# Performance work log

Measured on AMD Instinct MI355X. Metric: run time of the kernel, lower is better.

The kernel has to match this reference:

```python
import jax, jax.numpy as jnp
import numpy as np

RADII = (4, 8, 16)
BETA = 0.3
TEMP = 0.07
EPS = 1e-6


def box_filter(x, r):
    """Windowed sum over a (2r+1)x(2r+1) window with zero padding (same as
    F.conv2d with a ones kernel and padding=r), applied to the last two axes.
    Uses cumulative sums (integral image) instead of an explicit convolution."""
    def along(x, axis):
        n = x.shape[axis]
        c = jnp.cumsum(x, axis=axis)
        pad = [(0, 0)] * x.ndim
        pad[axis] = (1, 0)
        c = jnp.pad(c, pad)  # prepend a zero so c[i] = sum of first i elems
        i = jnp.arange(n)
        hi = jnp.clip(i + r + 1, 0, n)
        lo = jnp.clip(i - r, 0, n)
        return jnp.take(c, hi, axis=axis) - jnp.take(c, lo, axis=axis)
    return along(along(x, -2), -1)


def build_prototypes(support_feats, mask_f, anchor_pos, anchor_sample, anchor_radius):
    """mask_f: [S,H,W] float. Returns (local_protos [M,C], local_weights [M], global_proto [C])."""
    fg = mask_f.sum()
    global_proto = (support_feats * mask_f[:, None]).sum((0, 2, 3)) / (fg + EPS)

    masked = support_feats * mask_f[:, None]  # [S,C,H,W]
    means, msums = [], []
    for r in RADII:
        fsum = box_filter(masked, r)              # [S,C,H,W] windowed masked feature sum
        msum = box_filter(mask_f, r)              # [S,H,W]   windowed fg pixel count
        means.append(fsum / (msum[:, None] + EPS))
        msums.append(msum)
    mean = jnp.stack(means)   # [R,S,C,H,W] windowed masked means per radius
    msum = jnp.stack(msums)   # [R,S,H,W]

    y, x = anchor_pos[:, 0], anchor_pos[:, 1]
    local_protos = mean[anchor_radius, anchor_sample, :, y, x]   # [M,C]
    local_weights = msum[anchor_radius, anchor_sample, y, x]     # [M]
    local_weights = local_weights / (local_weights.sum() + EPS)
    return local_protos, local_weights, global_proto


def _l2norm(x, axis):
    n = jnp.sqrt(jnp.sum(x * x, axis=axis, keepdims=True))
    return x / jnp.maximum(n, 1e-12)


def reference(support_feats, support_masks, query_feats, anchor_pos, anchor_sample, anchor_radius):
    mask_f = support_masks.astype(support_feats.dtype)[:, 0]  # [S,H,W]
    protos, weights, gproto = build_prototypes(
        support_feats, mask_f, anchor_pos, anchor_sample, anchor_radius)

    q_norm = _l2norm(query_feats, axis=1)                     # [B,C,H,W]
    g = _l2norm(gproto[None], axis=1)[0]                      # [C]
    s_global = jnp.einsum('bchw,c->bhw', q_norm, g)

    p_norm = _l2norm(protos, axis=1)                          # [M,C]
    sims = jnp.einsum('bchw,mc->bmhw', q_norm, p_norm)        # [B,M,H,W]
    w = weights / (weights.sum() + EPS)
    local_score = jnp.einsum('bmhw,m->bhw', sims, w)

    s_fg = BETA * s_global + (1.0 - BETA) * local_score
    logits = jnp.stack((-s_fg / TEMP, s_fg / TEMP), axis=1)   # [B,2,H,W]
    return logits


def setup_inputs() -> dict:
    key = jax.random.key(0)
    k1, k2, k3, k4, k5, k6 = jax.random.split(key, 6)
    S, C, H, W = 4, 384, 96, 96
    B, M = 8, 64
    return {
        'support_feats': jax.random.normal(k1, (S, C, H, W), dtype=jnp.float32),
        'support_masks': jax.random.randint(k2, (S, 1, H, W), 0, 2, dtype=jnp.int32),
        'query_feats': jax.random.normal(k3, (B, C, H, W), dtype=jnp.float32),
        'anchor_pos': jax.random.randint(k4, (M, 2), 0, H, dtype=jnp.int32),
        'anchor_sample': jax.random.randint(k5, (M,), 0, S, dtype=jnp.int32),
        'anchor_radius': jax.random.randint(k6, (M,), 0, len(RADII), dtype=jnp.int32),
    }
```

## Files before the change

### kernel.cpp

```cpp
#include <hip/hip_runtime.h>
#include <hip/hip_bf16.h>
#include <math.h>

#define S_ 4
#define C_ 384
#define H_ 96
#define W_ 96
#define B_ 8
#define M_ 64
#define HW_ (H_ * W_)
#define EPSV 1e-6f
#define BETA_V 0.3f
#define TEMP_V 0.07f

__device__ __forceinline__ float wave_sum(float v) {
#pragma unroll
    for (int o = 32; o; o >>= 1) v += __shfl_down(v, o, 64);
    return v;
}

__device__ __forceinline__ float block_sum(float v) {
    __shared__ float sm[8];
    int lane = threadIdx.x & 63;
    int wid = threadIdx.x >> 6;
    v = wave_sum(v);
    if (lane == 0) sm[wid] = v;
    __syncthreads();
    int nw = blockDim.x >> 6;
    float r = 0.0f;
    for (int i = 0; i < nw; ++i) r += sm[i];
    __syncthreads();
    return r;
}

__global__ __launch_bounds__(256) void k_gpartial(const float* __restrict__ feats,
                                                  const int* __restrict__ mask,
                                                  float* __restrict__ partial) {
    int sc = blockIdx.x;
    int s = sc / C_;
    const float4* fp = (const float4*)(feats + (size_t)sc * HW_);
    const int4* mp = (const int4*)(mask + (size_t)s * HW_);
    float acc = 0.0f;
    for (int i = threadIdx.x; i < HW_ / 4; i += blockDim.x) {
        float4 f = fp[i];
        int4 m = mp[i];
        acc += f.x * (float)m.x + f.y * (float)m.y + f.z * (float)m.z + f.w * (float)m.w;
    }
    float tot = block_sum(acc);
    if (threadIdx.x == 0) partial[sc] = tot;
}

__global__ __launch_bounds__(256) void k_local(const float* __restrict__ feats,
                                               const int* __restrict__ mask,
                                               const int* __restrict__ pos,
                                               const int* __restrict__ samp,
                                               const int* __restrict__ rad,
                                               float* __restrict__ proto,
                                               float* __restrict__ msum_out) {
    const int CG = C_ / 4;
    int m = blockIdx.x / CG;
    int cg = blockIdx.x % CG;
    int y = pos[2 * m + 0];
    int x = pos[2 * m + 1];
    int s = samp[m];
    int ri = rad[m];
    int r = (ri == 0) ? 4 : (ri == 1) ? 8 : 16;
    int y0 = max(y - r, 0), y1 = min(y + r + 1, H_);
    int x0 = max(x - r, 0), x1 = min(x + r + 1, W_);
    int ww = x1 - x0;
    int n = (y1 - y0) * ww;

    __shared__ float mwin[33 * 33];
    const int* mp = mask + (size_t)s * HW_;
    float macc = 0.0f;
    for (int i = threadIdx.x; i < n; i += blockDim.x) {
        int yy = y0 + i / ww;
        int xx = x0 + i % ww;
        float mv = (float)mp[yy * W_ + xx];
        mwin[i] = mv;
        macc += mv;
    }
    float msum = block_sum(macc);
    if (cg == 0 && threadIdx.x == 0) msum_out[m] = msum;
    float inv = 1.0f / (msum + EPSV);

    int wid = threadIdx.x >> 6;
    int lane = threadIdx.x & 63;
    int c = cg * 4 + wid;
    const float* fp = feats + ((size_t)s * C_ + c) * HW_;
    float acc = 0.0f;
    for (int i = lane; i < n; i += 64) {
        int yy = y0 + i / ww;
        int xx = x0 + i % ww;
        acc += fp[yy * W_ + xx] * mwin[i];
    }
    acc = wave_sum(acc);
    if (lane == 0) proto[m * C_ + c] = acc * inv;
}

__global__ __launch_bounds__(256) void k_finalize(const int* __restrict__ mask,
                                                  const float* __restrict__ partial,
                                                  const float* __restrict__ msum,
                                                  const float* __restrict__ proto,
                                                  float* __restrict__ v) {
    int tid = threadIdx.x;
    int wid = tid >> 6;
    int lane = tid & 63;

    const int4* mp4 = (const int4*)mask;
    float acc = 0.0f;
    for (int i = tid; i < S_ * HW_ / 4; i += blockDim.x) {
        int4 m = mp4[i];
        acc += (float)(m.x + m.y + m.z + m.w);
    }
    float fg = block_sum(acc);
    float invfg = 1.0f / (fg + EPSV);

    __shared__ float gv[C_];
    for (int c = tid; c < C_; c += blockDim.x) {
        float t = 0.0f;
        for (int s = 0; s < S_; ++s) t += partial[s * C_ + c];
        gv[c] = t * invfg;
    }
    __syncthreads();

    float sq = 0.0f;
    for (int c = tid; c < C_; c += blockDim.x) sq += gv[c] * gv[c];
    float gn = block_sum(sq);
    gn = fmaxf(sqrtf(gn), 1e-12f);

    float wa = (tid < M_) ? msum[tid] : 0.0f;
    float T = block_sum(wa);
    float wb = (tid < M_) ? msum[tid] / (T + EPSV) : 0.0f;
    float wsum = block_sum(wb);

    __shared__ float pn[M_];
    for (int m = wid; m < M_; m += 4) {
        float a = 0.0f;
        for (int c = lane; c < C_; c += 64) {
            float p = proto[m * C_ + c];
            a += p * p;
        }
        a = wave_sum(a);
        if (lane == 0) pn[m] = fmaxf(sqrtf(a), 1e-12f);
    }
    __syncthreads();

    __shared__ float wq[M_];
    if (tid < M_) {
        float w = (msum[tid] / (T + EPSV)) / (wsum + EPSV);
        wq[tid] = w / pn[tid];
    }
    __syncthreads();

    for (int c = tid; c < C_; c += blockDim.x) {
        float vl = 0.0f;
        for (int m = 0; m < M_; ++m) vl += wq[m] * proto[m * C_ + c];
        v[c] = BETA_V * (gv[c] / gn) + (1.0f - BETA_V) * vl;
    }
}

__global__ __launch_bounds__(256) void k_score(const float* __restrict__ q,
                                               const float* __restrict__ v,
                                               float* __restrict__ out) {
    __shared__ float vs[C_];
    for (int c = threadIdx.x; c < C_; c += blockDim.x) vs[c] = v[c];
    __syncthreads();

    int wid = threadIdx.x >> 6;
    int lane = threadIdx.x & 63;
    int pixbase = blockIdx.x * 64;
    int b = pixbase / HW_;
    int p0 = pixbase - b * HW_;
    const float* qp = q + ((size_t)b * C_ + wid * 96) * HW_ + p0 + lane;

    float dot = 0.0f, sq = 0.0f;
#pragma unroll 8
    for (int c = 0; c < 96; ++c) {
        float val = qp[(size_t)c * HW_];
        dot += val * vs[wid * 96 + c];
        sq += val * val;
    }

    __shared__ float sdot[4][64];
    __shared__ float ssq[4][64];
    sdot[wid][lane] = dot;
    ssq[wid][lane] = sq;
    __syncthreads();
    if (wid == 0) {
        float d = sdot[0][lane] + sdot[1][lane] + sdot[2][lane] + sdot[3][lane];
        float s2 = ssq[0][lane] + ssq[1][lane] + ssq[2][lane] + ssq[3][lane];
        float sv = d / fmaxf(sqrtf(s2), 1e-12f);
        float o = sv / TEMP_V;
        float* ob = out + (size_t)b * 2 * HW_;
        ob[p0 + lane] = -o;
        ob[HW_ + p0 + lane] = o;
    }
}

extern "C" void kernel_launch(void* const* d_in, const int* in_sizes, int n_in,
                              void* d_out, int out_size, void* d_ws, size_t ws_size,
                              hipStream_t stream) {
    const float* support_feats = (const float*)d_in[0];
    const int* support_masks = (const int*)d_in[1];
    const float* query_feats = (const float*)d_in[2];
    const int* anchor_pos = (const int*)d_in[3];
    const int* anchor_sample = (const int*)d_in[4];
    const int* anchor_radius = (const int*)d_in[5];
    float* out = (float*)d_out;

    float* ws = (float*)d_ws;
    float* ws_partial = ws;
    float* ws_msum = ws_partial + S_ * C_;
    float* ws_proto = ws_msum + M_;
    float* ws_v = ws_proto + M_ * C_;

    k_gpartial<<<S_ * C_, 256, 0, stream>>>(support_feats, support_masks, ws_partial);
    k_local<<<M_ * (C_ / 4), 256, 0, stream>>>(support_feats, support_masks, anchor_pos,
                                               anchor_sample, anchor_radius, ws_proto, ws_msum);
    k_finalize<<<1, 256, 0, stream>>>(support_masks, ws_partial, ws_msum, ws_proto, ws_v);
    k_score<<<B_ * HW_ / 64, 256, 0, stream>>>(query_feats, ws_v, out);
}
```

Baseline: 98.43 us.

## Fuse prep kernels, move fg count off single block, vectorize score loads

Merges the global-partial and local-prototype kernels into one launch with block-index dispatch, and adds an extra block that computes the foreground count so the single-block finalize kernel no longer scans the whole mask. The local window loops replace per-element div/mod with incremental row/column stepping. The score kernel now has each thread handle four pixels through float4 loads and stores, using a quarter as many blocks. The cost is fewer score blocks and more registers per thread.

```diff
diff --git a/kernel.cpp b/kernel.cpp
--- a/kernel.cpp
+++ b/kernel.cpp
@@ -13,6 +13,10 @@
 #define BETA_V 0.3f
 #define TEMP_V 0.07f
 
+#define NB_A (S_ * C_)
+#define NB_B (M_ * (C_ / 4))
+#define NB_PREP (NB_A + NB_B + 1)
+
 __device__ __forceinline__ float wave_sum(float v) {
 #pragma unroll
     for (int o = 32; o; o >>= 1) v += __shfl_down(v, o, 64);
@@ -26,106 +30,123 @@
     v = wave_sum(v);
     if (lane == 0) sm[wid] = v;
     __syncthreads();
-    int nw = blockDim.x >> 6;
     float r = 0.0f;
-    for (int i = 0; i < nw; ++i) r += sm[i];
+#pragma unroll
+    for (int i = 0; i < 4; ++i) r += sm[i];
     __syncthreads();
     return r;
 }
 
-__global__ __launch_bounds__(256) void k_gpartial(const float* __restrict__ feats,
-                                                  const int* __restrict__ mask,
-                                                  float* __restrict__ partial) {
-    int sc = blockIdx.x;
-    int s = sc / C_;
-    const float4* fp = (const float4*)(feats + (size_t)sc * HW_);
-    const int4* mp = (const int4*)(mask + (size_t)s * HW_);
+__global__ __launch_bounds__(256) void k_prep(const float* __restrict__ feats,
+                                              const int* __restrict__ mask,
+                                              const int* __restrict__ pos,
+                                              const int* __restrict__ samp,
+                                              const int* __restrict__ rad,
+                                              float* __restrict__ partial,
+                                              float* __restrict__ proto,
+                                              float* __restrict__ msum_out,
+                                              float* __restrict__ fg_out) {
+    int bid = blockIdx.x;
+    int t = threadIdx.x;
+
+    if (bid < NB_A) {
+        int s = bid / C_;
+        const float4* fp = (const float4*)(feats + (size_t)bid * HW_);
+        const int4* mp = (const int4*)(mask + (size_t)s * HW_);
+        float acc = 0.0f;
+        for (int i = t; i < HW_ / 4; i += 256) {
+            float4 f = fp[i];
+            int4 m = mp[i];
+            acc += f.x * (float)m.x + f.y * (float)m.y + f.z * (float)m.z + f.w * (float)m.w;
+        }
+        float tot = block_sum(acc);
+        if (t == 0) partial[bid] = tot;
+        return;
+    }
+    bid -= NB_A;
+    if (bid < NB_B) {
+        const int CG = C_ / 4;
+        int m = bid / CG;
+        int cg = bid % CG;
+        int y = pos[2 * m + 0];
+        int x = pos[2 * m + 1];
+        int s = samp[m];
+        int ri = rad[m];
+        int r = (ri == 0) ? 4 : (ri == 1) ? 8 : 16;
+        int y0 = max(y - r, 0), y1 = min(y + r + 1, H_);
+        int x0 = max(x - r, 0), x1 = min(x + r + 1, W_);
+        int ww = x1 - x0;
+        int n = (y1 - y0) * ww;
+
+        __shared__ float mwin[33 * 33];
+        const int* mp = mask + (size_t)s * HW_;
+        float macc = 0.0f;
+        {
+            int yy = t / ww;
+            int xx = t - yy * ww;
+            int dy = 256 / ww, dx = 256 - dy * ww;
+            for (int i = t; i < n; i += 256) {
+                float mv = (float)mp[(y0 + yy) * W_ + x0 + xx];
+                mwin[i] = mv;
+                macc += mv;
+                xx += dx; yy += dy;
+                if (xx >= ww) { xx -= ww; ++yy; }
+            }
+        }
+        float msumv = block_sum(macc);
+        if (cg == 0 && t == 0) msum_out[m] = msumv;
+        float inv = 1.0f / (msumv + EPSV);
+
+        int wid = t >> 6;
+        int lane = t & 63;
+        int c = cg * 4 + wid;
+        const float* fp = feats + ((size_t)s * C_ + c) * HW_;
+        float acc = 0.0f;
+        {
+            int yy = lane / ww;
+            int xx = lane - yy * ww;
+            int dy = 64 / ww, dx = 64 - dy * ww;
+            for (int i = lane; i < n; i += 64) {
+                acc += fp[(y0 + yy) * W_ + x0 + xx] * mwin[i];
+                xx += dx; yy += dy;
+                if (xx >= ww) { xx -= ww; ++yy; }
+            }
+        }
+        acc = wave_sum(acc);
+        if (lane == 0) proto[m * C_ + c] = acc * inv;
+        return;
+    }
+    const int4* mp4 = (const int4*)mask;
     float acc = 0.0f;
-    for (int i = threadIdx.x; i < HW_ / 4; i += blockDim.x) {
-        float4 f = fp[i];
-        int4 m = mp[i];
-        acc += f.x * (float)m.x + f.y * (float)m.y + f.z * (float)m.z + f.w * (float)m.w;
-    }
-    float tot = block_sum(acc);
-    if (threadIdx.x == 0) partial[sc] = tot;
-}
-
-__global__ __launch_bounds__(256) void k_local(const float* __restrict__ feats,
-                                               const int* __restrict__ mask,
-                                               const int* __restrict__ pos,
-                                               const int* __restrict__ samp,
-                                               const int* __restrict__ rad,
-                                               float* __restrict__ proto,
-                                               float* __restrict__ msum_out) {
-    const int CG = C_ / 4;
-    int m = blockIdx.x / CG;
-    int cg = blockIdx.x % CG;
-    int y = pos[2 * m + 0];
-    int x = pos[2 * m + 1];
-    int s = samp[m];
-    int ri = rad[m];
-    int r = (ri == 0) ? 4 : (ri == 1) ? 8 : 16;
-    int y0 = max(y - r, 0), y1 = min(y + r + 1, H_);
-    int x0 = max(x - r, 0), x1 = min(x + r + 1, W_);
-    int ww = x1 - x0;
-    int n = (y1 - y0) * ww;
-
-    __shared__ float mwin[33 * 33];
-    const int* mp = mask + (size_t)s * HW_;
-    float macc = 0.0f;
-    for (int i = threadIdx.x; i < n; i += blockDim.x) {
-        int yy = y0 + i / ww;
-        int xx = x0 + i % ww;
-        float mv = (float)mp[yy * W_ + xx];
-        mwin[i] = mv;
-        macc += mv;
-    }
-    float msum = block_sum(macc);
-    if (cg == 0 && threadIdx.x == 0) msum_out[m] = msum;
-    float inv = 1.0f / (msum + EPSV);
-
-    int wid = threadIdx.x >> 6;
-    int lane = threadIdx.x & 63;
-    int c = cg * 4 + wid;
-    const float* fp = feats + ((size_t)s * C_ + c) * HW_;
-    float acc = 0.0f;
-    for (int i = lane; i < n; i += 64) {
-        int yy = y0 + i / ww;
-        int xx = x0 + i % ww;
-        acc += fp[yy * W_ + xx] * mwin[i];
-    }
-    acc = wave_sum(acc);
-    if (lane == 0) proto[m * C_ + c] = acc * inv;
-}
-
-__global__ __launch_bounds__(256) void k_finalize(const int* __restrict__ mask,
-                                                  const float* __restrict__ partial,
+    for (int i = t; i < S_ * HW_ / 4; i += 256) {
+        int4 m = mp4[i];
+        acc += (float)(m.x + m.y + m.z + m.w);
+    }
+    float fg = block_sum(acc);
+    if (t == 0) fg_out[0] = fg;
+}
+
+__global__ __launch_bounds__(256) void k_finalize(const float* __restrict__ partial,
                                                   const float* __restrict__ msum,
                                                   const float* __restrict__ proto,
+                                                  const float* __restrict__ fg_in,
                                                   float* __restrict__ v) {
     int tid = threadIdx.x;
     int wid = tid >> 6;
     int lane = tid & 63;
 
-    const int4* mp4 = (const int4*)mask;
-    float acc = 0.0f;
-    for (int i = tid; i < S_ * HW_ / 4; i += blockDim.x) {
-        int4 m = mp4[i];
-        acc += (float)(m.x + m.y + m.z + m.w);
-    }
-    float fg = block_sum(acc);
-    float invfg = 1.0f / (fg + EPSV);
+    float invfg = 1.0f / (fg_in[0] + EPSV);
 
     __shared__ float gv[C_];
-    for (int c = tid; c < C_; c += blockDim.x) {
-        float t = 0.0f;
-        for (int s = 0; s < S_; ++s) t += partial[s * C_ + c];
-        gv[c] = t * invfg;
+    for (int c = tid; c < C_; c += 256) {
+        float tv = 0.0f;
+        for (int s = 0; s < S_; ++s) tv += partial[s * C_ + c];
+        gv[c] = tv * invfg;
     }
     __syncthreads();
 
     float sq = 0.0f;
-    for (int c = tid; c < C_; c += blockDim.x) sq += gv[c] * gv[c];
+    for (int c = tid; c < C_; c += 256) sq += gv[c] * gv[c];
     float gn = block_sum(sq);
     gn = fmaxf(sqrtf(gn), 1e-12f);
 
@@ -153,7 +174,7 @@
     }
     __syncthreads();
 
-    for (int c = tid; c < C_; c += blockDim.x) {
+    for (int c = tid; c < C_; c += 256) {
         float vl = 0.0f;
         for (int m = 0; m < M_; ++m) vl += wq[m] * proto[m * C_ + c];
         v[c] = BETA_V * (gv[c] / gn) + (1.0f - BETA_V) * vl;
@@ -164,37 +185,50 @@
                                                const float* __restrict__ v,
                                                float* __restrict__ out) {
     __shared__ float vs[C_];
-    for (int c = threadIdx.x; c < C_; c += blockDim.x) vs[c] = v[c];
+    for (int c = threadIdx.x; c < C_; c += 256) vs[c] = v[c];
     __syncthreads();
 
     int wid = threadIdx.x >> 6;
     int lane = threadIdx.x & 63;
-    int pixbase = blockIdx.x * 64;
+    int pixbase = blockIdx.x * 256;
     int b = pixbase / HW_;
     int p0 = pixbase - b * HW_;
-    const float* qp = q + ((size_t)b * C_ + wid * 96) * HW_ + p0 + lane;
-
-    float dot = 0.0f, sq = 0.0f;
+    const float4* qp = (const float4*)(q + ((size_t)b * C_ + wid * 96) * HW_ + p0);
+
+    float4 dot = {0.f, 0.f, 0.f, 0.f};
+    float4 sq = {0.f, 0.f, 0.f, 0.f};
 #pragma unroll 8
     for (int c = 0; c < 96; ++c) {
-        float val = qp[(size_t)c * HW_];
-        dot += val * vs[wid * 96 + c];
-        sq += val * val;
-    }
-
-    __shared__ float sdot[4][64];
-    __shared__ float ssq[4][64];
-    sdot[wid][lane] = dot;
-    ssq[wid][lane] = sq;
+        float4 f = qp[(size_t)c * (HW_ / 4) + lane];
+        float vc = vs[wid * 96 + c];
+        dot.x += f.x * vc; dot.y += f.y * vc; dot.z += f.z * vc; dot.w += f.w * vc;
+        sq.x += f.x * f.x; sq.y += f.y * f.y; sq.z += f.z * f.z; sq.w += f.w * f.w;
+    }
+
+    __shared__ float4 sd[4][64];
+    __shared__ float4 ss[4][64];
+    sd[wid][lane] = dot;
+    ss[wid][lane] = sq;
     __syncthreads();
     if (wid == 0) {
-        float d = sdot[0][lane] + sdot[1][lane] + sdot[2][lane] + sdot[3][lane];
-        float s2 = ssq[0][lane] + ssq[1][lane] + ssq[2][lane] + ssq[3][lane];
-        float sv = d / fmaxf(sqrtf(s2), 1e-12f);
-        float o = sv / TEMP_V;
+        float4 d = sd[0][lane];
+        float4 s2 = ss[0][lane];
+#pragma unroll
+        for (int w = 1; w < 4; ++w) {
+            float4 a = sd[w][lane];
+            float4 b2 = ss[w][lane];
+            d.x += a.x; d.y += a.y; d.z += a.z; d.w += a.w;
+            s2.x += b2.x; s2.y += b2.y; s2.z += b2.z; s2.w += b2.w;
+        }
+        float4 o;
+        o.x = (d.x / fmaxf(sqrtf(s2.x), 1e-12f)) / TEMP_V;
+        o.y = (d.y / fmaxf(sqrtf(s2.y), 1e-12f)) / TEMP_V;
+        o.z = (d.z / fmaxf(sqrtf(s2.z), 1e-12f)) / TEMP_V;
+        o.w = (d.w / fmaxf(sqrtf(s2.w), 1e-12f)) / TEMP_V;
+        float4 no = {-o.x, -o.y, -o.z, -o.w};
         float* ob = out + (size_t)b * 2 * HW_;
-        ob[p0 + lane] = -o;
-        ob[HW_ + p0 + lane] = o;
+        ((float4*)(ob + p0))[lane] = no;
+        ((float4*)(ob + HW_ + p0))[lane] = o;
     }
 }
 
@@ -214,10 +248,11 @@
     float* ws_msum = ws_partial + S_ * C_;
     float* ws_proto = ws_msum + M_;
     float* ws_v = ws_proto + M_ * C_;
-
-    k_gpartial<<<S_ * C_, 256, 0, stream>>>(support_feats, support_masks, ws_partial);
-    k_local<<<M_ * (C_ / 4), 256, 0, stream>>>(support_feats, support_masks, anchor_pos,
-                                               anchor_sample, anchor_radius, ws_proto, ws_msum);
-    k_finalize<<<1, 256, 0, stream>>>(support_masks, ws_partial, ws_msum, ws_proto, ws_v);
-    k_score<<<B_ * HW_ / 64, 256, 0, stream>>>(query_feats, ws_v, out);
-}
+    float* ws_fg = ws_v + C_;
+
+    k_prep<<<NB_PREP, 256, 0, stream>>>(support_feats, support_masks, anchor_pos,
+                                        anchor_sample, anchor_radius,
+                                        ws_partial, ws_proto, ws_msum, ws_fg);
+    k_finalize<<<1, 256, 0, stream>>>(ws_partial, ws_msum, ws_proto, ws_fg, ws_v);
+    k_score<<<B_ * HW_ / 256, 256, 0, stream>>>(query_feats, ws_v, out);
+}
```

New measurement: 95.97 us. 2.5% less time.
